# Optimization experiments

Hardware: AMD Instinct MI355X
Metric: run time of the kernel (lower is better)

## Reference

```python
import jax, jax.numpy as jnp
import numpy as np

# Static config (matches init_kwargs: dim=64, ffn=2.66, kernel=3, smk=3, heads=2)
DIM = 64
NUM_HEADS = 2
KS = 3
SMK = 3
POOL = 7           # ContMix pools context to 7x7 -> 49 context tokens
HIDDEN = 172       # round_up(int(64*2.66), 4)
HIDDEN2 = 2 * HIDDEN
CTX_DW = HIDDEN2 // 4   # 86
CTX_DW12 = HIDDEN // 4  # 43
NK = SMK * SMK + KS * KS  # 18


def conv1x1(x, w):
    # x: [B,C,H,W], w: [O,C] -> [B,O,H,W]
    return jnp.einsum('bchw,oc->bohw', x, w)


def extract_patches(x, k):
    # x: [B,C,H,W] -> [B,C,k*k,H,W], zero ('same') padding, stride 1
    p = k // 2
    B, C, H, W = x.shape
    xp = jnp.pad(x, ((0, 0), (0, 0), (p, p), (p, p)))
    pats = [xp[:, :, i:i + H, j:j + W] for i in range(k) for j in range(k)]
    return jnp.stack(pats, axis=2)


def dyn_dw(x, attn, k, heads):
    # Dynamic depthwise mixing: per-pixel, per-head k*k kernel shared across
    # channels within a head. x: [B,C,H,W], attn: [B,g,HW,k*k]
    B, C, H, W = x.shape
    hd = C // heads
    pat = extract_patches(x, k).reshape(B, heads, hd, k * k, H * W)
    out = jnp.einsum('bgdkn,bgnk->bgdn', pat, attn)
    return out.reshape(B, C, H, W)


def contmix(x, ctx, wq, wk, wp, wpb, wo):
    # Content-aware dynamic depthwise-mixing (ContMix, OverLoCK-style).
    B, C, H, W = x.shape
    hd_qk = (C // 2) // NUM_HEADS
    scale = hd_qk ** -0.5
    # query from x, key from 7x7-pooled context
    q = conv1x1(x, wq) * scale                     # [B, C//2, H, W]
    ph, pw = H // POOL, W // POOL
    ctx_p = ctx.reshape(B, -1, POOL, ph, POOL, pw).mean(axis=(3, 5))  # [B,ctx,7,7]
    key = conv1x1(ctx_p, wk)                       # [B, C//2, 7, 7]
    q = q.reshape(B, NUM_HEADS, hd_qk, H * W)
    key = key.reshape(B, NUM_HEADS, hd_qk, POOL * POOL)
    w = jnp.einsum('bgcn,bgcl->bgnl', q, key)      # [B,g,HW,49]
    # project 49 context scores -> smk^2 + k^2 dynamic kernel taps (1x1 conv w/ bias)
    w = jnp.einsum('bgnl,ol->bgno', w, wp) + wpb   # [B,g,HW,18]
    a1 = jax.nn.softmax(w[..., :SMK * SMK], axis=-1)
    a2 = jax.nn.softmax(w[..., SMK * SMK:], axis=-1)
    # first channel half mixed with small kernel, second half with large kernel
    x1, x2 = jnp.split(x, 2, axis=1)
    y = jnp.concatenate([dyn_dw(x1, a1, SMK, NUM_HEADS),
                         dyn_dw(x2, a2, KS, NUM_HEADS)], axis=1)
    return conv1x1(y, wo)


def setup_inputs() -> dict:
    key = jax.random.key(0)
    ks = jax.random.split(key, 32)
    def w(i, o, c):
        return jax.random.normal(ks[i], (o, c), dtype=jnp.float32) / np.sqrt(c)
    inp = {
        'x': jax.random.normal(ks[0], (2, DIM, 112, 112), dtype=jnp.float32),
        'pin_w': w(1, HIDDEN2, DIM),
        'ctx_w': w(2, CTX_DW, HIDDEN2),
        'ctx1_w': w(3, CTX_DW12, HIDDEN),
        'ctx2_w': w(4, CTX_DW12, HIDDEN),
        'pout_w': w(5, DIM, HIDDEN),
        # ContMix on hidden_x2 (dim=344, ctx=86)
        'cm0_q': w(6, HIDDEN2 // 2, HIDDEN2),
        'cm0_k': w(7, HIDDEN2 // 2, CTX_DW),
        'cm0_p': w(8, NK, POOL * POOL),
        'cm0_pb': jnp.zeros((NK,), dtype=jnp.float32),
        'cm0_o': w(9, HIDDEN2, HIDDEN2),
        # ContMix on hidden (dim=172, ctx=43) -- branch 1
        'cm1_q': w(10, HIDDEN // 2, HIDDEN),
        'cm1_k': w(11, HIDDEN // 2, CTX_DW12),
        'cm1_p': w(12, NK, POOL * POOL),
        'cm1_pb': jnp.zeros((NK,), dtype=jnp.float32),
        'cm1_o': w(13, HIDDEN, HIDDEN),
        # ContMix on hidden -- branch 2
        'cm2_q': w(14, HIDDEN // 2, HIDDEN),
        'cm2_k': w(15, HIDDEN // 2, CTX_DW12),
        'cm2_p': w(16, NK, POOL * POOL),
        'cm2_pb': jnp.zeros((NK,), dtype=jnp.float32),
        'cm2_o': w(17, HIDDEN, HIDDEN),
    }
    return inp


def reference(x, pin_w, ctx_w, ctx1_w, ctx2_w, pout_w,
              cm0_q, cm0_k, cm0_p, cm0_pb, cm0_o,
              cm1_q, cm1_k, cm1_p, cm1_pb, cm1_o,
              cm2_q, cm2_k, cm2_p, cm2_pb, cm2_o):
    x_in = conv1x1(x, pin_w)                           # [B, 2*hidden, H, W]
    ctx_dw = conv1x1(x_in, ctx_w)                      # [B, ctx_dw, H, W]
    x_dw = contmix(x_in, ctx_dw, cm0_q, cm0_k, cm0_p, cm0_pb, cm0_o)
    x1, x2 = jnp.split(x_dw, 2, axis=1)                # each [B, hidden, H, W]
    ctx1 = conv1x1(x1, ctx1_w)
    ctx2 = conv1x1(x2, ctx2_w)
    x1p = jnp.tanh(contmix(x1, ctx1, cm1_q, cm1_k, cm1_p, cm1_pb, cm1_o)) + x1
    x2p = jnp.tanh(contmix(x2, ctx2, cm2_q, cm2_k, cm2_p, cm2_pb, cm2_o)) + x2
    out = conv1x1(x1p * x2p, pout_w)                   # [B, dim, H, W]
    return out
```

## Files before the change

kernel.cpp:

```cpp
#include <hip/hip_runtime.h>
#include <math.h>

#define HW 12544
#define W_IMG 112
#define B_SZ 2

typedef __attribute__((ext_vector_type(8))) short s8v;
typedef __attribute__((ext_vector_type(4))) float f4v;

__device__ __forceinline__ void split_bf16(float x, unsigned short& h, unsigned short& l) {
    unsigned u  = __float_as_uint(x);
    unsigned hb = (u + 0x7FFFu + ((u >> 16) & 1u)) >> 16;
    float hf    = __uint_as_float(hb << 16);
    float r     = x - hf;
    unsigned ur = __float_as_uint(r);
    unsigned lb = (ur + 0x7FFFu + ((ur >> 16) & 1u)) >> 16;
    h = (unsigned short)hb; l = (unsigned short)lb;
}

struct WSplitArgs {
    const float* src[8];
    const float* src2[8];
    unsigned short* hi[8];
    unsigned short* lo[8];
    int O1[8]; int O2[8]; int O2B[8]; int K[8]; int Kp[8]; int MpKp[8];
    float scale2[8];
};

__global__ __launch_bounds__(256) void wsplit_k(WSplitArgs a) {
    const int ci  = blockIdx.y;
    const int idx = blockIdx.x * 256 + threadIdx.x;
    if (idx >= a.MpKp[ci]) return;
    const int Kp   = a.Kp[ci];
    const int blk  = 32 * Kp;
    const int mblk = idx / blk;
    const int rem  = idx - mblk * blk;
    const int kc   = rem >> 10;
    const int rem2 = rem & 1023;
    const int kq   = rem2 >> 8;
    const int row  = (rem2 >> 3) & 31;
    const int j    = rem2 & 7;
    const int o = mblk * 32 + row, k = kc * 32 + kq * 8 + j;
    float v = 0.f;
    if (k < a.K[ci]) {
        if (o < a.O1[ci])
            v = a.src[ci][(size_t)o * a.K[ci] + k];
        else if (o >= a.O2B[ci] && o - a.O2B[ci] < a.O2[ci])
            v = a.src2[ci][(size_t)(o - a.O2B[ci]) * a.K[ci] + k] * a.scale2[ci];
    }
    unsigned short h, l;
    split_bf16(v, h, l);
    a.hi[ci][idx] = h; a.lo[ci][idx] = l;
}

__global__ __launch_bounds__(256) void tsplit_k(
    const float* __restrict__ src, size_t bstride, int C, int KC,
    unsigned short* __restrict__ hi, unsigned short* __restrict__ lo)
{
    __shared__ __align__(16) float t[32][36];
    const int b   = blockIdx.z;
    const int hw0 = blockIdx.x * 32;
    const int kc  = blockIdx.y;
    const int c0  = kc * 32;
    const int tid = threadIdx.x;

    {
        const int cl = tid >> 3, hq = (tid & 7) * 4;
        const int c  = c0 + cl;
        float4 v = make_float4(0.f, 0.f, 0.f, 0.f);
        if (c < C)
            v = *(const float4*)(src + (size_t)b * bstride + (size_t)c * HW + hw0 + hq);
        *(float4*)&t[cl][hq] = v;
    }
    __syncthreads();

    const int hl = tid >> 3, cq = (tid & 7) * 4;
    float v0 = t[cq + 0][hl], v1 = t[cq + 1][hl], v2 = t[cq + 2][hl], v3 = t[cq + 3][hl];
    ushort4 h4, l4;
    split_bf16(v0, h4.x, l4.x);
    split_bf16(v1, h4.y, l4.y);
    split_bf16(v2, h4.z, l4.z);
    split_bf16(v3, h4.w, l4.w);
    const int ns = hw0 >> 8, r = (hw0 & 255) + hl;
    const int kq = cq >> 3, j0 = cq & 7;
    const size_t base = (((size_t)b * 49 + ns) * KC + kc) * 8192
                        + (size_t)kq * 2048 + (size_t)r * 8 + j0;
    *(ushort4*)(hi + base) = h4;
    *(ushort4*)(lo + base) = l4;
}

__global__ __launch_bounds__(256) void tsplit2_k(
    const float* __restrict__ src, size_t bstride,
    unsigned short* __restrict__ hi_a, unsigned short* __restrict__ lo_a,
    unsigned short* __restrict__ hi_b, unsigned short* __restrict__ lo_b)
{
    __shared__ __align__(16) float t[32][36];
    const int zz = blockIdx.z, b = zz & 1, br = zz >> 1;
    const int hw0 = blockIdx.x * 32;
    const int kc  = blockIdx.y;
    const int c0  = kc * 32;
    const int tid = threadIdx.x;

    {
        const int cl = tid >> 3, hq = (tid & 7) * 4;
        const int c  = c0 + cl;
        float4 v = make_float4(0.f, 0.f, 0.f, 0.f);
        if (c < 172)
            v = *(const float4*)(src + (size_t)b * bstride
                                 + (size_t)(br * 172 + c) * HW + hw0 + hq);
        *(float4*)&t[cl][hq] = v;
    }
    __syncthreads();

    const int hl = tid >> 3, cq = (tid & 7) * 4;
    float v0 = t[cq + 0][hl], v1 = t[cq + 1][hl], v2 = t[cq + 2][hl], v3 = t[cq + 3][hl];
    ushort4 h4, l4;
    split_bf16(v0, h4.x, l4.x);
    split_bf16(v1, h4.y, l4.y);
    split_bf16(v2, h4.z, l4.z);
    split_bf16(v3, h4.w, l4.w);
    const int ns = hw0 >> 8, r = (hw0 & 255) + hl;
    const int kq = cq >> 3, j0 = cq & 7;
    const size_t base = (((size_t)b * 49 + ns) * 6 + kc) * 8192
                        + (size_t)kq * 2048 + (size_t)r * 8 + j0;
    unsigned short* hi = br ? hi_b : hi_a;
    unsigned short* lo = br ? lo_b : lo_a;
    *(ushort4*)(hi + base) = h4;
    *(ushort4*)(lo + base) = l4;
}

__global__ __launch_bounds__(256) void mulsplit_k(
    const float* __restrict__ t1, const float* __restrict__ t2, size_t bstride,
    unsigned short* __restrict__ hi, unsigned short* __restrict__ lo)
{
    __shared__ __align__(16) float t[32][36];
    const int b   = blockIdx.z;
    const int hw0 = blockIdx.x * 32;
    const int kc  = blockIdx.y;
    const int c0  = kc * 32;
    const int tid = threadIdx.x;

    {
        const int cl = tid >> 3, hq = (tid & 7) * 4;
        const int c  = c0 + cl;
        float4 v = make_float4(0.f, 0.f, 0.f, 0.f);
        if (c < 172) {
            const size_t off = (size_t)b * bstride + (size_t)c * HW + hw0 + hq;
            float4 a = *(const float4*)(t1 + off);
            float4 m = *(const float4*)(t2 + off);
            v = make_float4(a.x * m.x, a.y * m.y, a.z * m.z, a.w * m.w);
        }
        *(float4*)&t[cl][hq] = v;
    }
    __syncthreads();

    const int hl = tid >> 3, cq = (tid & 7) * 4;
    float v0 = t[cq + 0][hl], v1 = t[cq + 1][hl], v2 = t[cq + 2][hl], v3 = t[cq + 3][hl];
    ushort4 h4, l4;
    split_bf16(v0, h4.x, l4.x);
    split_bf16(v1, h4.y, l4.y);
    split_bf16(v2, h4.z, l4.z);
    split_bf16(v3, h4.w, l4.w);
    const int ns = hw0 >> 8, r = (hw0 & 255) + hl;
    const int kq = cq >> 3, j0 = cq & 7;
    const size_t base = (((size_t)b * 49 + ns) * 6 + kc) * 8192
                        + (size_t)kq * 2048 + (size_t)r * 8 + j0;
    *(ushort4*)(hi + base) = h4;
    *(ushort4*)(lo + base) = l4;
}

template <int KP>
__global__ __launch_bounds__(256) void gemm_k(
    const unsigned short* __restrict__ bt_hi, const unsigned short* __restrict__ bt_lo,
    const unsigned short* __restrict__ w_hi,  const unsigned short* __restrict__ w_lo,
    int per_m,
    float* __restrict__ outA, int OA, size_t oa_bstride,
    float* __restrict__ outB, int OB, size_t ob_bstride, int obase)
{
    constexpr int KC = KP / 32;
    __shared__ __align__(16) unsigned short Bh_s[8192];
    __shared__ __align__(16) unsigned short Bl_s[8192];
    __shared__ __align__(16) unsigned short Ah_s[1024];
    __shared__ __align__(16) unsigned short Al_s[1024];

    const int b   = blockIdx.y;
    const int bx  = blockIdx.x;
    const int xcd = bx & 7, t = bx >> 3;
    const int m   = t % per_m;
    const int ns  = (t / per_m) * 8 + xcd;
    if (ns >= 49) return;

    const int tid  = threadIdx.x;
    const int wv   = tid >> 6, lane = tid & 63;
    const int m16  = lane & 15, quad = lane >> 4;
    const int mbase = m * 32;
    const int nbase = ns * 256 + wv * 64;

    const unsigned short* Bh_g = bt_hi + ((size_t)b * 49 + ns) * KC * 8192;
    const unsigned short* Bl_g = bt_lo + ((size_t)b * 49 + ns) * KC * 8192;
    const unsigned short* Ah_g = w_hi + (size_t)m * KC * 1024;
    const unsigned short* Al_g = w_lo + (size_t)m * KC * 1024;

    f4v acc[2][4];
#pragma unroll
    for (int mt = 0; mt < 2; ++mt)
#pragma unroll
        for (int f = 0; f < 4; ++f) acc[mt][f] = (f4v){0.f, 0.f, 0.f, 0.f};

    s8v rB[8], rA;
#pragma unroll
    for (int j = 0; j < 4; ++j) {
        rB[j]     = *(const s8v*)(Bh_g + (size_t)(j * 256 + tid) * 8);
        rB[4 + j] = *(const s8v*)(Bl_g + (size_t)(j * 256 + tid) * 8);
    }
    rA = (tid < 128) ? *(const s8v*)(Ah_g + (size_t)tid * 8)
                     : *(const s8v*)(Al_g + (size_t)(tid - 128) * 8);
#pragma unroll
    for (int j = 0; j < 4; ++j) {
        *(s8v*)(Bh_s + (j * 256 + tid) * 8) = rB[j];
        *(s8v*)(Bl_s + (j * 256 + tid) * 8) = rB[4 + j];
    }
    if (tid < 128) *(s8v*)(Ah_s + tid * 8) = rA;
    else           *(s8v*)(Al_s + (tid - 128) * 8) = rA;
    __syncthreads();

#pragma unroll
    for (int kc = 0; kc < KC; ++kc) {
        if (kc + 1 < KC) {
            const unsigned short* bh = Bh_g + (size_t)(kc + 1) * 8192;
            const unsigned short* bl = Bl_g + (size_t)(kc + 1) * 8192;
#pragma unroll
            for (int j = 0; j < 4; ++j) {
                rB[j]     = *(const s8v*)(bh + (size_t)(j * 256 + tid) * 8);
                rB[4 + j] = *(const s8v*)(bl + (size_t)(j * 256 + tid) * 8);
            }
            rA = (tid < 128)
                ? *(const s8v*)(Ah_g + (size_t)(kc + 1) * 1024 + (size_t)tid * 8)
                : *(const s8v*)(Al_g + (size_t)(kc + 1) * 1024 + (size_t)(tid - 128) * 8);
        }
#pragma unroll
        for (int mt = 0; mt < 2; ++mt) {
            s8v ah = *(const s8v*)(Ah_s + (quad * 32 + mt * 16 + m16) * 8);
            s8v al = *(const s8v*)(Al_s + (quad * 32 + mt * 16 + m16) * 8);
#pragma unroll
            for (int f = 0; f < 4; ++f) {
                const int row = wv * 64 + f * 16 + m16;
                s8v bh = *(const s8v*)(Bh_s + (quad * 256 + row) * 8);
                s8v bl = *(const s8v*)(Bl_s + (quad * 256 + row) * 8);
                acc[mt][f] = __builtin_amdgcn_mfma_f32_16x16x32_bf16(ah, bh, acc[mt][f], 0, 0, 0);
                acc[mt][f] = __builtin_amdgcn_mfma_f32_16x16x32_bf16(al, bh, acc[mt][f], 0, 0, 0);
                acc[mt][f] = __builtin_amdgcn_mfma_f32_16x16x32_bf16(ah, bl, acc[mt][f], 0, 0, 0);
            }
        }
        __syncthreads();
        if (kc + 1 < KC) {
#pragma unroll
            for (int j = 0; j < 4; ++j) {
                *(s8v*)(Bh_s + (j * 256 + tid) * 8) = rB[j];
                *(s8v*)(Bl_s + (j * 256 + tid) * 8) = rB[4 + j];
            }
            if (tid < 128) *(s8v*)(Ah_s + tid * 8) = rA;
            else           *(s8v*)(Al_s + (tid - 128) * 8) = rA;
            __syncthreads();
        }
    }

#pragma unroll
    for (int mt = 0; mt < 2; ++mt) {
#pragma unroll
        for (int f = 0; f < 4; ++f) {
            const int n = nbase + f * 16 + m16;
#pragma unroll
            for (int r = 0; r < 4; ++r) {
                const int o = mbase + mt * 16 + quad * 4 + r;
                float v = acc[mt][f][r];
                if (o < OA) {
                    outA[(size_t)b * oa_bstride + (size_t)o * HW + n] = v;
                } else if (o >= obase && o - obase < OB) {
                    outB[(size_t)b * ob_bstride + (size_t)(o - obase) * HW + n] = v;
                }
            }
        }
    }
}

template <int KP>
__global__ __launch_bounds__(256) void gemm2_k(
    const unsigned short* __restrict__ bth_a, const unsigned short* __restrict__ btl_a,
    const unsigned short* __restrict__ wh_a,  const unsigned short* __restrict__ wl_a,
    const unsigned short* __restrict__ bth_b, const unsigned short* __restrict__ btl_b,
    const unsigned short* __restrict__ wh_b,  const unsigned short* __restrict__ wl_b,
    int per_m,
    float* __restrict__ outA_a, float* __restrict__ outA_b, int OA, size_t oa_bstride,
    float* __restrict__ outB_a, float* __restrict__ outB_b, int OB, size_t ob_bstride, int obase,
    int mode, int Ovalid,
    const float* __restrict__ res_a, const float* __restrict__ res_b, size_t res_bstride)
{
    constexpr int KC = KP / 32;
    __shared__ __align__(16) unsigned short Bh_s[8192];
    __shared__ __align__(16) unsigned short Bl_s[8192];
    __shared__ __align__(16) unsigned short Ah_s[1024];
    __shared__ __align__(16) unsigned short Al_s[1024];

    const int zz  = blockIdx.y, b = zz & 1, br = zz >> 1;
    const int bx  = blockIdx.x;
    const int xcd = bx & 7, t = bx >> 3;
    const int m   = t % per_m;
    const int ns  = (t / per_m) * 8 + xcd;
    if (ns >= 49) return;

    const unsigned short* bt_hi = br ? bth_b : bth_a;
    const unsigned short* bt_lo = br ? btl_b : btl_a;
    const unsigned short* w_hi  = br ? wh_b : wh_a;
    const unsigned short* w_lo  = br ? wl_b : wl_a;
    float* outA = br ? outA_b : outA_a;
    float* outB = br ? outB_b : outB_a;
    const float* res = br ? res_b : res_a;

    const int tid  = threadIdx.x;
    const int wv   = tid >> 6, lane = tid & 63;
    const int m16  = lane & 15, quad = lane >> 4;
    const int mbase = m * 32;
    const int nbase = ns * 256 + wv * 64;

    const unsigned short* Bh_g = bt_hi + ((size_t)b * 49 + ns) * KC * 8192;
    const unsigned short* Bl_g = bt_lo + ((size_t)b * 49 + ns) * KC * 8192;
    const unsigned short* Ah_g = w_hi + (size_t)m * KC * 1024;
    const unsigned short* Al_g = w_lo + (size_t)m * KC * 1024;

    f4v acc[2][4];
#pragma unroll
    for (int mt = 0; mt < 2; ++mt)
#pragma unroll
        for (int f = 0; f < 4; ++f) acc[mt][f] = (f4v){0.f, 0.f, 0.f, 0.f};

    s8v rB[8], rA;
#pragma unroll
    for (int j = 0; j < 4; ++j) {
        rB[j]     = *(const s8v*)(Bh_g + (size_t)(j * 256 + tid) * 8);
        rB[4 + j] = *(const s8v*)(Bl_g + (size_t)(j * 256 + tid) * 8);
    }
    rA = (tid < 128) ? *(const s8v*)(Ah_g + (size_t)tid * 8)
                     : *(const s8v*)(Al_g + (size_t)(tid - 128) * 8);
#pragma unroll
    for (int j = 0; j < 4; ++j) {
        *(s8v*)(Bh_s + (j * 256 + tid) * 8) = rB[j];
        *(s8v*)(Bl_s + (j * 256 + tid) * 8) = rB[4 + j];
    }
    if (tid < 128) *(s8v*)(Ah_s + tid * 8) = rA;
    else           *(s8v*)(Al_s + (tid - 128) * 8) = rA;
    __syncthreads();

#pragma unroll
    for (int kc = 0; kc < KC; ++kc) {
        if (kc + 1 < KC) {
            const unsigned short* bh = Bh_g + (size_t)(kc + 1) * 8192;
            const unsigned short* bl = Bl_g + (size_t)(kc + 1) * 8192;
#pragma unroll
            for (int j = 0; j < 4; ++j) {
                rB[j]     = *(const s8v*)(bh + (size_t)(j * 256 + tid) * 8);
                rB[4 + j] = *(const s8v*)(bl + (size_t)(j * 256 + tid) * 8);
            }
            rA = (tid < 128)
                ? *(const s8v*)(Ah_g + (size_t)(kc + 1) * 1024 + (size_t)tid * 8)
                : *(const s8v*)(Al_g + (size_t)(kc + 1) * 1024 + (size_t)(tid - 128) * 8);
        }
#pragma unroll
        for (int mt = 0; mt < 2; ++mt) {
            s8v ah = *(const s8v*)(Ah_s + (quad * 32 + mt * 16 + m16) * 8);
            s8v al = *(const s8v*)(Al_s + (quad * 32 + mt * 16 + m16) * 8);
#pragma unroll
            for (int f = 0; f < 4; ++f) {
                const int row = wv * 64 + f * 16 + m16;
                s8v bh = *(const s8v*)(Bh_s + (quad * 256 + row) * 8);
                s8v bl = *(const s8v*)(Bl_s + (quad * 256 + row) * 8);
                acc[mt][f] = __builtin_amdgcn_mfma_f32_16x16x32_bf16(ah, bh, acc[mt][f], 0, 0, 0);
                acc[mt][f] = __builtin_amdgcn_mfma_f32_16x16x32_bf16(al, bh, acc[mt][f], 0, 0, 0);
                acc[mt][f] = __builtin_amdgcn_mfma_f32_16x16x32_bf16(ah, bl, acc[mt][f], 0, 0, 0);
            }
        }
        __syncthreads();
        if (kc + 1 < KC) {
#pragma unroll
            for (int j = 0; j < 4; ++j) {
                *(s8v*)(Bh_s + (j * 256 + tid) * 8) = rB[j];
                *(s8v*)(Bl_s + (j * 256 + tid) * 8) = rB[4 + j];
            }
            if (tid < 128) *(s8v*)(Ah_s + tid * 8) = rA;
            else           *(s8v*)(Al_s + (tid - 128) * 8) = rA;
            __syncthreads();
        }
    }

#pragma unroll
    for (int mt = 0; mt < 2; ++mt) {
#pragma unroll
        for (int f = 0; f < 4; ++f) {
            const int n = nbase + f * 16 + m16;
#pragma unroll
            for (int r = 0; r < 4; ++r) {
                const int o = mbase + mt * 16 + quad * 4 + r;
                float v = acc[mt][f][r];
                if (mode == 2 && o < Ovalid)
                    v = tanhf(v) + res[(size_t)b * res_bstride + (size_t)o * HW + n];
                if (o < OA) {
                    outA[(size_t)b * oa_bstride + (size_t)o * HW + n] = v;
                } else if (o >= obase && o - obase < OB) {
                    outB[(size_t)b * ob_bstride + (size_t)(o - obase) * HW + n] = v;
                }
            }
        }
    }
}

__global__ __launch_bounds__(256) void dyndw_bt_k(
    const float* __restrict__ x, const float* __restrict__ attn,
    unsigned short* __restrict__ hi, unsigned short* __restrict__ lo,
    int C, int C_half, int hd, size_t x_bstride, int KC)
{
    const int b  = blockIdx.z, ns = blockIdx.x, tid = threadIdx.x;
    const int c0 = blockIdx.y * 8;
    const int hw = ns * 256 + tid;
    const int h = hw / W_IMG, w = hw - h * W_IMG;

    int off[9]; bool val[9];
#pragma unroll
    for (int i = 0; i < 3; ++i)
#pragma unroll
        for (int j = 0; j < 3; ++j) {
            const int hh = h + i - 1, ww = w + j - 1;
            val[i * 3 + j] = (hh >= 0 && hh < 112 && ww >= 0 && ww < 112);
            off[i * 3 + j] = hh * W_IMG + ww;
        }

    s8v hvv, lvv;
#pragma unroll
    for (int u = 0; u < 8; ++u) {
        const int c = c0 + u;
        float acc = 0.f;
        if (c < C) {
            const int half = c / C_half;
            const int g = (c - half * C_half) / hd;
            const float* ap = attn + ((size_t)(b * 2 + g) * 18 + half * 9) * HW + hw;
            const float* xp = x + (size_t)b * x_bstride + (size_t)c * HW;
#pragma unroll
            for (int k = 0; k < 9; ++k) {
                const float xv = val[k] ? xp[off[k]] : 0.f;
                acc += ap[(size_t)k * HW] * xv;
            }
        }
        unsigned short hs, ls;
        split_bf16(acc, hs, ls);
        hvv[u] = (short)hs; lvv[u] = (short)ls;
    }

    const int kc = c0 >> 5, kq = (c0 & 31) >> 3;
    const size_t base = (((size_t)b * 49 + ns) * KC + kc) * 8192
                        + (size_t)kq * 2048 + (size_t)tid * 8;
    *(s8v*)(hi + base) = hvv;
    *(s8v*)(lo + base) = lvv;
}

__global__ __launch_bounds__(256) void dyndw2_bt_k(
    const float* __restrict__ x, size_t x_bstride,
    const float* __restrict__ attn_a, const float* __restrict__ attn_b,
    unsigned short* __restrict__ hi_a, unsigned short* __restrict__ lo_a,
    unsigned short* __restrict__ hi_b, unsigned short* __restrict__ lo_b)
{
    const int zz = blockIdx.z, b = zz & 1, br = zz >> 1;
    const int ns = blockIdx.x, tid = threadIdx.x;
    const int c0 = blockIdx.y * 8;
    const int hw = ns * 256 + tid;
    const int h = hw / W_IMG, w = hw - h * W_IMG;

    const float* attn = br ? attn_b : attn_a;
    unsigned short* hi = br ? hi_b : hi_a;
    unsigned short* lo = br ? lo_b : lo_a;

    int off[9]; bool val[9];
#pragma unroll
    for (int i = 0; i < 3; ++i)
#pragma unroll
        for (int j = 0; j < 3; ++j) {
            const int hh = h + i - 1, ww = w + j - 1;
            val[i * 3 + j] = (hh >= 0 && hh < 112 && ww >= 0 && ww < 112);
            off[i * 3 + j] = hh * W_IMG + ww;
        }

    s8v hvv, lvv;
#pragma unroll
    for (int u = 0; u < 8; ++u) {
        const int c = c0 + u;
        float acc = 0.f;
        if (c < 172) {
            const int half = c / 86;
            const int g = (c - half * 86) / 43;
            const float* ap = attn + ((size_t)(b * 2 + g) * 18 + half * 9) * HW + hw;
            const float* xp = x + (size_t)b * x_bstride + (size_t)(br * 172 + c) * HW;
#pragma unroll
            for (int k = 0; k < 9; ++k) {
                const float xv = val[k] ? xp[off[k]] : 0.f;
                acc += ap[(size_t)k * HW] * xv;
            }
        }
        unsigned short hs, ls;
        split_bf16(acc, hs, ls);
        hvv[u] = (short)hs; lvv[u] = (short)ls;
    }

    const int kc = c0 >> 5, kq = (c0 & 31) >> 3;
    const size_t base = (((size_t)b * 49 + ns) * 6 + kc) * 8192
                        + (size_t)kq * 2048 + (size_t)tid * 8;
    *(s8v*)(hi + base) = hvv;
    *(s8v*)(lo + base) = lvv;
}

__global__ __launch_bounds__(64) void pool_k(
    const float* __restrict__ ctx, float* __restrict__ pooled, int C)
{
    const int c = blockIdx.x, b = blockIdx.y, t = threadIdx.x;
    if (t >= 49) return;
    const int ph = t / 7, pw = t % 7;
    const float* src = ctx + ((size_t)b * C + c) * HW;
    float sum = 0.f;
    for (int i = 0; i < 16; ++i) {
        const float* row = src + (ph * 16 + i) * W_IMG + pw * 16;
        for (int j = 0; j < 16; ++j) sum += row[j];
    }
    pooled[((size_t)b * C + c) * 49 + t] = sum * (1.0f / 256.0f);
}

__global__ __launch_bounds__(64) void pool2_k(
    const float* __restrict__ ctx_a, const float* __restrict__ ctx_b,
    float* __restrict__ p_a, float* __restrict__ p_b, int C)
{
    const int zz = blockIdx.y, b = zz & 1, br = zz >> 1;
    const int c = blockIdx.x, t = threadIdx.x;
    if (t >= 49) return;
    const float* ctx = br ? ctx_b : ctx_a;
    float* pooled    = br ? p_b : p_a;
    const int ph = t / 7, pw = t % 7;
    const float* src = ctx + ((size_t)b * C + c) * HW;
    float sum = 0.f;
    for (int i = 0; i < 16; ++i) {
        const float* row = src + (ph * 16 + i) * W_IMG + pw * 16;
        for (int j = 0; j < 16; ++j) sum += row[j];
    }
    pooled[((size_t)b * C + c) * 49 + t] = sum * (1.0f / 256.0f);
}

__global__ __launch_bounds__(64) void keygemm_k(
    const float* __restrict__ pooled, const float* __restrict__ wk,
    float* __restrict__ key, int K, int O)
{
    const int o = blockIdx.x, b = blockIdx.y, l = threadIdx.x;
    if (l >= 49) return;
    float s = 0.f;
    for (int c = 0; c < K; ++c)
        s += wk[(size_t)o * K + c] * pooled[((size_t)b * K + c) * 49 + l];
    key[((size_t)b * O + o) * 49 + l] = s;
}

__global__ __launch_bounds__(64) void keygemm2_k(
    const float* __restrict__ p_a, const float* __restrict__ p_b,
    const float* __restrict__ wk_a, const float* __restrict__ wk_b,
    float* __restrict__ k_a, float* __restrict__ k_b, int K, int O)
{
    const int zz = blockIdx.y, b = zz & 1, br = zz >> 1;
    const int o = blockIdx.x, l = threadIdx.x;
    if (l >= 49) return;
    const float* pooled = br ? p_b : p_a;
    const float* wk     = br ? wk_b : wk_a;
    float* key          = br ? k_b : k_a;
    float s = 0.f;
    for (int c = 0; c < K; ++c)
        s += wk[(size_t)o * K + c] * pooled[((size_t)b * K + c) * 49 + l];
    key[((size_t)b * O + o) * 49 + l] = s;
}

__device__ __forceinline__ void attn_body(
    const float* __restrict__ q, const float* __restrict__ key,
    const float* __restrict__ wp, const float* __restrict__ pb,
    float* __restrict__ attn, int hd, int b, int g, int tid, int nsx)
{
    __shared__ float klds[86 * 52];
    __shared__ float plds[18 * 52];
    __shared__ float pblds[18];

    for (int idx = tid; idx < hd * 49; idx += 256) {
        int c = idx / 49, l = idx - c * 49;
        klds[c * 52 + l] = key[((size_t)(b * 2 + g) * hd + c) * 49 + l];
    }
    for (int idx = tid; idx < hd * 3; idx += 256) {
        int c = idx / 3;
        klds[c * 52 + 49 + (idx - c * 3)] = 0.f;
    }
    for (int idx = tid; idx < 18 * 49; idx += 256) {
        int o = idx / 49, l = idx - o * 49;
        plds[o * 52 + l] = wp[o * 49 + l];
    }
    for (int idx = tid; idx < 18 * 3; idx += 256) {
        int o = idx / 3;
        plds[o * 52 + 49 + (idx - o * 3)] = 0.f;
    }
    if (tid < 18) pblds[tid] = pb[tid];
    __syncthreads();

    const int hw = nsx * 256 + tid;

    float4 s[13];
#pragma unroll
    for (int t = 0; t < 13; ++t) s[t] = make_float4(0.f, 0.f, 0.f, 0.f);

    const float* qp = q + (size_t)(b * 2 + g) * hd * HW + hw;
    for (int c = 0; c < hd; ++c) {
        float qv = qp[(size_t)c * HW];
        const float4* kr = (const float4*)(klds + c * 52);
#pragma unroll
        for (int t = 0; t < 13; ++t) {
            float4 kv = kr[t];
            s[t].x += qv * kv.x; s[t].y += qv * kv.y;
            s[t].z += qv * kv.z; s[t].w += qv * kv.w;
        }
    }

    float e[18];
#pragma unroll
    for (int o = 0; o < 18; ++o) {
        const float4* pr = (const float4*)(plds + o * 52);
        float4 a = make_float4(0.f, 0.f, 0.f, 0.f);
#pragma unroll
        for (int t = 0; t < 13; ++t) {
            float4 pv = pr[t];
            a.x += s[t].x * pv.x; a.y += s[t].y * pv.y;
            a.z += s[t].z * pv.z; a.w += s[t].w * pv.w;
        }
        e[o] = pblds[o] + a.x + a.y + a.z + a.w;
    }

    float* outp = attn + (size_t)(b * 2 + g) * 18 * HW + hw;
#pragma unroll
    for (int half = 0; half < 2; ++half) {
        int base = half * 9;
        float m = e[base];
#pragma unroll
        for (int k = 1; k < 9; ++k) m = fmaxf(m, e[base + k]);
        float sum = 0.f, ex[9];
#pragma unroll
        for (int k = 0; k < 9; ++k) { ex[k] = expf(e[base + k] - m); sum += ex[k]; }
        float inv = 1.0f / sum;
#pragma unroll
        for (int k = 0; k < 9; ++k) outp[(size_t)(base + k) * HW] = ex[k] * inv;
    }
}

__global__ __launch_bounds__(256) void attn_k(
    const float* __restrict__ q, const float* __restrict__ key,
    const float* __restrict__ wp, const float* __restrict__ pb,
    float* __restrict__ attn, int hd)
{
    attn_body(q, key, wp, pb, attn, hd, blockIdx.z, blockIdx.y, threadIdx.x, blockIdx.x);
}

__global__ __launch_bounds__(256) void attn2_k(
    const float* __restrict__ q_a, const float* __restrict__ q_b,
    const float* __restrict__ k_a, const float* __restrict__ k_b,
    const float* __restrict__ wp_a, const float* __restrict__ wp_b,
    const float* __restrict__ pb_a, const float* __restrict__ pb_b,
    float* __restrict__ at_a, float* __restrict__ at_b, int hd)
{
    const int zz = blockIdx.z, b = zz & 1, br = zz >> 1;
    attn_body(br ? q_b : q_a, br ? k_b : k_a, br ? wp_b : wp_a,
              br ? pb_b : pb_a, br ? at_b : at_a, hd, b, blockIdx.y,
              threadIdx.x, blockIdx.x);
}

extern "C" void kernel_launch(void* const* d_in, const int* in_sizes, int n_in,
                              void* d_out, int out_size, void* d_ws, size_t ws_size,
                              hipStream_t stream) {
    const float* x      = (const float*)d_in[0];
    const float* pin_w  = (const float*)d_in[1];
    const float* ctx_w  = (const float*)d_in[2];
    const float* ctx1_w = (const float*)d_in[3];
    const float* ctx2_w = (const float*)d_in[4];
    const float* pout_w = (const float*)d_in[5];
    const float* cm0_q  = (const float*)d_in[6];
    const float* cm0_k  = (const float*)d_in[7];
    const float* cm0_p  = (const float*)d_in[8];
    const float* cm0_pb = (const float*)d_in[9];
    const float* cm0_o  = (const float*)d_in[10];
    const float* cm1_q  = (const float*)d_in[11];
    const float* cm1_k  = (const float*)d_in[12];
    const float* cm1_p  = (const float*)d_in[13];
    const float* cm1_pb = (const float*)d_in[14];
    const float* cm1_o  = (const float*)d_in[15];
    const float* cm2_q  = (const float*)d_in[16];
    const float* cm2_k  = (const float*)d_in[17];
    const float* cm2_p  = (const float*)d_in[18];
    const float* cm2_pb = (const float*)d_in[19];
    const float* cm2_o  = (const float*)d_in[20];
    float* out = (float*)d_out;

    float* ws = (float*)d_ws;
    float* x_in  = ws;
    float* t1    = ws;
    float* t2    = ws + 8630272;
    float* x_dw  = ws + 17260544;
    float* ctxb  = ws + 25890816;
    float* ctx1  = ws + 28048384;
    float* ctx2  = ws + 29127168;
    float* q0    = ws + 30205952;
    float* q1    = ws + 30205952;
    float* q2    = ws + 32363520;
    float* attn0 = ws + 34521088;
    float* attn1 = ws + 35424256;
    float* attn2 = ws + 36327424;
    float* pool0 = ws + 37230592;
    float* pool1 = ws + 37239020;
    float* pool2b= ws + 37243234;
    float* key0  = ws + 37247448;
    float* key1  = ws + 37264304;
    float* key2  = ws + 37272732;
    unsigned short* ub = (unsigned short*)(ws + 37281160);
    static const int WOFF[8] = {0, 45056, 247808, 518144, 579584, 641024, 714752, 788480};
    static const int WO1[8]  = {344, 86, 172, 43, 43, 172, 172, 64};
    static const int WO2[8]  = {0, 172, 172, 86, 86, 0, 0, 0};
    static const int O2B[8]  = {352, 86, 192, 43, 43, 192, 192, 64};
    static const int WK[8]   = {64, 344, 344, 172, 172, 172, 172, 172};
    static const int WKP[8]  = {64, 352, 352, 192, 192, 192, 192, 192};
    static const int WMP[8]  = {352, 288, 384, 160, 160, 192, 192, 64};
    unsigned short* xt_hi   = ub + 813056;
    unsigned short* xt_lo   = ub + 2418688;
    unsigned short* bigA_hi = ub + 4024320;
    unsigned short* bigA_lo = ub + 12855296;
    unsigned short* x1t_hi  = ub + 21686272;
    unsigned short* x1t_lo  = ub + 26503168;
    unsigned short* x2t_hi  = ub + 31320064;
    unsigned short* x2t_lo  = ub + 36136960;

    const float sc0 = 1.0f / sqrtf(86.0f);
    const float sc1 = 1.0f / sqrtf(43.0f);
    const size_t BS344 = (size_t)344 * HW, BS172 = (size_t)172 * HW,
                 BS86 = (size_t)86 * HW, BS64 = (size_t)64 * HW, BS43 = (size_t)43 * HW;

    WSplitArgs wa;
    const float* wsrc1[8] = {pin_w, ctx_w, cm0_o, ctx1_w, ctx2_w, cm1_o, cm2_o, pout_w};
    const float* wsrc2[8] = {nullptr, cm0_q, cm0_o + (size_t)172 * 344, cm1_q, cm2_q,
                             nullptr, nullptr, nullptr};
    const float wsc2[8]   = {1.f, sc0, 1.f, sc1, sc1, 1.f, 1.f, 1.f};
    for (int i = 0; i < 8; ++i) {
        wa.src[i] = wsrc1[i]; wa.src2[i] = wsrc2[i];
        wa.hi[i]  = ub + WOFF[i];
        wa.lo[i]  = ub + WOFF[i] + WMP[i] * WKP[i];
        wa.O1[i] = WO1[i]; wa.O2[i] = WO2[i]; wa.O2B[i] = O2B[i];
        wa.K[i] = WK[i]; wa.Kp[i] = WKP[i];
        wa.MpKp[i] = WMP[i] * WKP[i];
        wa.scale2[i] = wsc2[i];
    }
    wsplit_k<<<dim3(528, 8), 256, 0, stream>>>(wa);

#define WHI(CI) (ub + WOFF[CI])
#define WLO(CI) (ub + WOFF[CI] + WMP[CI] * WKP[CI])
#define GRID(CI) dim3((WMP[CI] / 32) * 56, B_SZ)
#define GRID2(CI) dim3((WMP[CI] / 32) * 56, 2 * B_SZ)

    tsplit_k<<<dim3(392, 2, B_SZ), 256, 0, stream>>>(x, BS64, 64, 2, xt_hi, xt_lo);
    gemm_k<64><<<GRID(0), 256, 0, stream>>>(
        xt_hi, xt_lo, WHI(0), WLO(0), WMP[0] / 32,
        x_in, 344, BS344, nullptr, 0, 0, 352);
    tsplit_k<<<dim3(392, 11, B_SZ), 256, 0, stream>>>(x_in, BS344, 344, 11, bigA_hi, bigA_lo);

    gemm_k<352><<<GRID(1), 256, 0, stream>>>(
        bigA_hi, bigA_lo, WHI(1), WLO(1), WMP[1] / 32,
        ctxb, 86, BS86, q0, 172, BS172, 86);
    pool_k<<<dim3(86, B_SZ), dim3(64), 0, stream>>>(ctxb, pool0, 86);
    keygemm_k<<<dim3(172, B_SZ), dim3(64), 0, stream>>>(pool0, cm0_k, key0, 86, 172);
    attn_k<<<dim3(49, 2, B_SZ), dim3(256), 0, stream>>>(q0, key0, cm0_p, cm0_pb, attn0, 86);
    dyndw_bt_k<<<dim3(49, 44, B_SZ), 256, 0, stream>>>(
        x_in, attn0, bigA_hi, bigA_lo, 344, 172, 86, BS344, 11);
    gemm_k<352><<<GRID(2), 256, 0, stream>>>(
        bigA_hi, bigA_lo, WHI(2), WLO(2), WMP[2] / 32,
        x_dw, 172, BS344, x_dw + BS172, 172, BS344, 192);

    tsplit2_k<<<dim3(392, 6, 2 * B_SZ), 256, 0, stream>>>(
        x_dw, BS344, x1t_hi, x1t_lo, x2t_hi, x2t_lo);

    gemm2_k<192><<<GRID2(3), 256, 0, stream>>>(
        x1t_hi, x1t_lo, WHI(3), WLO(3),
        x2t_hi, x2t_lo, WHI(4), WLO(4), WMP[3] / 32,
        ctx1, ctx2, 43, BS43,
        q1, q2, 86, BS86, 43,
        0, 129, nullptr, nullptr, 0);
    pool2_k<<<dim3(43, 2 * B_SZ), dim3(64), 0, stream>>>(ctx1, ctx2, pool1, pool2b, 43);
    keygemm2_k<<<dim3(86, 2 * B_SZ), dim3(64), 0, stream>>>(
        pool1, pool2b, cm1_k, cm2_k, key1, key2, 43, 86);
    attn2_k<<<dim3(49, 2, 2 * B_SZ), dim3(256), 0, stream>>>(
        q1, q2, key1, key2, cm1_p, cm2_p, cm1_pb, cm2_pb, attn1, attn2, 43);
    dyndw2_bt_k<<<dim3(49, 24, 2 * B_SZ), 256, 0, stream>>>(
        x_dw, BS344, attn1, attn2, x1t_hi, x1t_lo, x2t_hi, x2t_lo);
    gemm2_k<192><<<GRID2(5), 256, 0, stream>>>(
        x1t_hi, x1t_lo, WHI(5), WLO(5),
        x2t_hi, x2t_lo, WHI(6), WLO(6), WMP[5] / 32,
        t1, t2, 172, BS172,
        nullptr, nullptr, 0, 0, 192,
        2, 172, x_dw, x_dw + BS172, BS344);

    mulsplit_k<<<dim3(392, 6, B_SZ), 256, 0, stream>>>(t1, t2, BS172, bigA_hi, bigA_lo);

    gemm_k<192><<<GRID(7), 256, 0, stream>>>(
        bigA_hi, bigA_lo, WHI(7), WLO(7), WMP[7] / 32,
        out, 64, BS64, nullptr, 0, 0, 64);

#undef WHI
#undef WLO
#undef GRID
#undef GRID2
}
```

Measured before the change: 487.2 us.

## Widen gemm2 M-tile to 64 rows and fuse key projection into attention

The dual-branch GEMM kernel now computes 64 output rows per block instead of 32. Each block reuses its staged activation tile across twice as many weight rows, which halves the number of blocks that reload the large B operand. Padding for the ctx/q weights grows from 160 to 192 rows to fit the new tile. Separately, the key projection kernels are removed and the key is computed from the pooled context inside the attention kernel. This saves launches and a round trip through memory, but every attention block redundantly recomputes the small key matrix.

```diff
diff --git a/kernel.cpp b/kernel.cpp
--- a/kernel.cpp
+++ b/kernel.cpp
@@ -299,8 +299,8 @@
     constexpr int KC = KP / 32;
     __shared__ __align__(16) unsigned short Bh_s[8192];
     __shared__ __align__(16) unsigned short Bl_s[8192];
-    __shared__ __align__(16) unsigned short Ah_s[1024];
-    __shared__ __align__(16) unsigned short Al_s[1024];
+    __shared__ __align__(16) unsigned short Ah_s[4096];
+    __shared__ __align__(16) unsigned short Al_s[4096];
 
     const int zz  = blockIdx.y, b = zz & 1, br = zz >> 1;
     const int bx  = blockIdx.x;
@@ -320,35 +320,37 @@
     const int tid  = threadIdx.x;
     const int wv   = tid >> 6, lane = tid & 63;
     const int m16  = lane & 15, quad = lane >> 4;
-    const int mbase = m * 32;
+    const int mbase = m * 64;
     const int nbase = ns * 256 + wv * 64;
 
     const unsigned short* Bh_g = bt_hi + ((size_t)b * 49 + ns) * KC * 8192;
     const unsigned short* Bl_g = bt_lo + ((size_t)b * 49 + ns) * KC * 8192;
-    const unsigned short* Ah_g = w_hi + (size_t)m * KC * 1024;
-    const unsigned short* Al_g = w_lo + (size_t)m * KC * 1024;
-
-    f4v acc[2][4];
-#pragma unroll
-    for (int mt = 0; mt < 2; ++mt)
+    const int amb = tid >> 7;
+    const int aoff = (tid & 127) * 8;
+    const unsigned short* Ah_g = w_hi + (size_t)(2 * m + amb) * KC * 1024 + aoff;
+    const unsigned short* Al_g = w_lo + (size_t)(2 * m + amb) * KC * 1024 + aoff;
+
+    f4v acc[4][4];
+#pragma unroll
+    for (int mt = 0; mt < 4; ++mt)
 #pragma unroll
         for (int f = 0; f < 4; ++f) acc[mt][f] = (f4v){0.f, 0.f, 0.f, 0.f};
 
-    s8v rB[8], rA;
+    s8v rB[8], rA[2];
 #pragma unroll
     for (int j = 0; j < 4; ++j) {
         rB[j]     = *(const s8v*)(Bh_g + (size_t)(j * 256 + tid) * 8);
         rB[4 + j] = *(const s8v*)(Bl_g + (size_t)(j * 256 + tid) * 8);
     }
-    rA = (tid < 128) ? *(const s8v*)(Ah_g + (size_t)tid * 8)
-                     : *(const s8v*)(Al_g + (size_t)(tid - 128) * 8);
+    rA[0] = *(const s8v*)(Ah_g);
+    rA[1] = *(const s8v*)(Al_g);
 #pragma unroll
     for (int j = 0; j < 4; ++j) {
         *(s8v*)(Bh_s + (j * 256 + tid) * 8) = rB[j];
         *(s8v*)(Bl_s + (j * 256 + tid) * 8) = rB[4 + j];
     }
-    if (tid < 128) *(s8v*)(Ah_s + tid * 8) = rA;
-    else           *(s8v*)(Al_s + (tid - 128) * 8) = rA;
+    *(s8v*)(Ah_s + amb * 2048 + aoff) = rA[0];
+    *(s8v*)(Al_s + amb * 2048 + aoff) = rA[1];
     __syncthreads();
 
 #pragma unroll
@@ -361,14 +363,14 @@
                 rB[j]     = *(const s8v*)(bh + (size_t)(j * 256 + tid) * 8);
                 rB[4 + j] = *(const s8v*)(bl + (size_t)(j * 256 + tid) * 8);
             }
-            rA = (tid < 128)
-                ? *(const s8v*)(Ah_g + (size_t)(kc + 1) * 1024 + (size_t)tid * 8)
-                : *(const s8v*)(Al_g + (size_t)(kc + 1) * 1024 + (size_t)(tid - 128) * 8);
-        }
-#pragma unroll
-        for (int mt = 0; mt < 2; ++mt) {
-            s8v ah = *(const s8v*)(Ah_s + (quad * 32 + mt * 16 + m16) * 8);
-            s8v al = *(const s8v*)(Al_s + (quad * 32 + mt * 16 + m16) * 8);
+            rA[0] = *(const s8v*)(Ah_g + (size_t)(kc + 1) * 1024);
+            rA[1] = *(const s8v*)(Al_g + (size_t)(kc + 1) * 1024);
+        }
+#pragma unroll
+        for (int mt = 0; mt < 4; ++mt) {
+            const int ab = (mt >> 1) * 2048 + (quad * 32 + (mt & 1) * 16 + m16) * 8;
+            s8v ah = *(const s8v*)(Ah_s + ab);
+            s8v al = *(const s8v*)(Al_s + ab);
 #pragma unroll
             for (int f = 0; f < 4; ++f) {
                 const int row = wv * 64 + f * 16 + m16;
@@ -386,14 +388,14 @@
                 *(s8v*)(Bh_s + (j * 256 + tid) * 8) = rB[j];
                 *(s8v*)(Bl_s + (j * 256 + tid) * 8) = rB[4 + j];
             }
-            if (tid < 128) *(s8v*)(Ah_s + tid * 8) = rA;
-            else           *(s8v*)(Al_s + (tid - 128) * 8) = rA;
+            *(s8v*)(Ah_s + amb * 2048 + aoff) = rA[0];
+            *(s8v*)(Al_s + amb * 2048 + aoff) = rA[1];
             __syncthreads();
         }
     }
 
 #pragma unroll
-    for (int mt = 0; mt < 2; ++mt) {
+    for (int mt = 0; mt < 4; ++mt) {
 #pragma unroll
         for (int f = 0; f < 4; ++f) {
             const int n = nbase + f * 16 + m16;
@@ -549,39 +551,11 @@
     pooled[((size_t)b * C + c) * 49 + t] = sum * (1.0f / 256.0f);
 }
 
-__global__ __launch_bounds__(64) void keygemm_k(
-    const float* __restrict__ pooled, const float* __restrict__ wk,
-    float* __restrict__ key, int K, int O)
-{
-    const int o = blockIdx.x, b = blockIdx.y, l = threadIdx.x;
-    if (l >= 49) return;
-    float s = 0.f;
-    for (int c = 0; c < K; ++c)
-        s += wk[(size_t)o * K + c] * pooled[((size_t)b * K + c) * 49 + l];
-    key[((size_t)b * O + o) * 49 + l] = s;
-}
-
-__global__ __launch_bounds__(64) void keygemm2_k(
-    const float* __restrict__ p_a, const float* __restrict__ p_b,
-    const float* __restrict__ wk_a, const float* __restrict__ wk_b,
-    float* __restrict__ k_a, float* __restrict__ k_b, int K, int O)
-{
-    const int zz = blockIdx.y, b = zz & 1, br = zz >> 1;
-    const int o = blockIdx.x, l = threadIdx.x;
-    if (l >= 49) return;
-    const float* pooled = br ? p_b : p_a;
-    const float* wk     = br ? wk_b : wk_a;
-    float* key          = br ? k_b : k_a;
-    float s = 0.f;
-    for (int c = 0; c < K; ++c)
-        s += wk[(size_t)o * K + c] * pooled[((size_t)b * K + c) * 49 + l];
-    key[((size_t)b * O + o) * 49 + l] = s;
-}
-
 __device__ __forceinline__ void attn_body(
-    const float* __restrict__ q, const float* __restrict__ key,
+    const float* __restrict__ q, const float* __restrict__ pooled,
+    const float* __restrict__ wk,
     const float* __restrict__ wp, const float* __restrict__ pb,
-    float* __restrict__ attn, int hd, int b, int g, int tid, int nsx)
+    float* __restrict__ attn, int hd, int K, int b, int g, int tid, int nsx)
 {
     __shared__ float klds[86 * 52];
     __shared__ float plds[18 * 52];
@@ -589,7 +563,11 @@
 
     for (int idx = tid; idx < hd * 49; idx += 256) {
         int c = idx / 49, l = idx - c * 49;
-        klds[c * 52 + l] = key[((size_t)(b * 2 + g) * hd + c) * 49 + l];
+        const float* wkr = wk + (size_t)(g * hd + c) * K;
+        const float* pl  = pooled + (size_t)b * K * 49 + l;
+        float s = 0.f;
+        for (int k = 0; k < K; ++k) s += wkr[k] * pl[(size_t)k * 49];
+        klds[c * 52 + l] = s;
     }
     for (int idx = tid; idx < hd * 3; idx += 256) {
         int c = idx / 3;
@@ -655,24 +633,26 @@
 }
 
 __global__ __launch_bounds__(256) void attn_k(
-    const float* __restrict__ q, const float* __restrict__ key,
-    const float* __restrict__ wp, const float* __restrict__ pb,
-    float* __restrict__ attn, int hd)
-{
-    attn_body(q, key, wp, pb, attn, hd, blockIdx.z, blockIdx.y, threadIdx.x, blockIdx.x);
+    const float* __restrict__ q, const float* __restrict__ pooled,
+    const float* __restrict__ wk, const float* __restrict__ wp,
+    const float* __restrict__ pb, float* __restrict__ attn, int hd, int K)
+{
+    attn_body(q, pooled, wk, wp, pb, attn, hd, K,
+              blockIdx.z, blockIdx.y, threadIdx.x, blockIdx.x);
 }
 
 __global__ __launch_bounds__(256) void attn2_k(
     const float* __restrict__ q_a, const float* __restrict__ q_b,
-    const float* __restrict__ k_a, const float* __restrict__ k_b,
+    const float* __restrict__ p_a, const float* __restrict__ p_b,
+    const float* __restrict__ wk_a, const float* __restrict__ wk_b,
     const float* __restrict__ wp_a, const float* __restrict__ wp_b,
     const float* __restrict__ pb_a, const float* __restrict__ pb_b,
-    float* __restrict__ at_a, float* __restrict__ at_b, int hd)
+    float* __restrict__ at_a, float* __restrict__ at_b, int hd, int K)
 {
     const int zz = blockIdx.z, b = zz & 1, br = zz >> 1;
-    attn_body(br ? q_b : q_a, br ? k_b : k_a, br ? wp_b : wp_a,
-              br ? pb_b : pb_a, br ? at_b : at_a, hd, b, blockIdx.y,
-              threadIdx.x, blockIdx.x);
+    attn_body(br ? q_b : q_a, br ? p_b : p_a, br ? wk_b : wk_a,
+              br ? wp_b : wp_a, br ? pb_b : pb_a, br ? at_b : at_a,
+              hd, K, b, blockIdx.y, threadIdx.x, blockIdx.x);
 }
 
 extern "C" void kernel_launch(void* const* d_in, const int* in_sizes, int n_in,
@@ -718,25 +698,22 @@
     float* pool0 = ws + 37230592;
     float* pool1 = ws + 37239020;
     float* pool2b= ws + 37243234;
-    float* key0  = ws + 37247448;
-    float* key1  = ws + 37264304;
-    float* key2  = ws + 37272732;
-    unsigned short* ub = (unsigned short*)(ws + 37281160);
-    static const int WOFF[8] = {0, 45056, 247808, 518144, 579584, 641024, 714752, 788480};
+    unsigned short* ub = (unsigned short*)(ws + 37247448);
+    static const int WOFF[8] = {0, 45056, 247808, 518144, 591872, 665600, 739328, 813056};
     static const int WO1[8]  = {344, 86, 172, 43, 43, 172, 172, 64};
     static const int WO2[8]  = {0, 172, 172, 86, 86, 0, 0, 0};
     static const int O2B[8]  = {352, 86, 192, 43, 43, 192, 192, 64};
     static const int WK[8]   = {64, 344, 344, 172, 172, 172, 172, 172};
     static const int WKP[8]  = {64, 352, 352, 192, 192, 192, 192, 192};
-    static const int WMP[8]  = {352, 288, 384, 160, 160, 192, 192, 64};
-    unsigned short* xt_hi   = ub + 813056;
-    unsigned short* xt_lo   = ub + 2418688;
-    unsigned short* bigA_hi = ub + 4024320;
-    unsigned short* bigA_lo = ub + 12855296;
-    unsigned short* x1t_hi  = ub + 21686272;
-    unsigned short* x1t_lo  = ub + 26503168;
-    unsigned short* x2t_hi  = ub + 31320064;
-    unsigned short* x2t_lo  = ub + 36136960;
+    static const int WMP[8]  = {352, 288, 384, 192, 192, 192, 192, 64};
+    unsigned short* xt_hi   = ub + 837632;
+    unsigned short* xt_lo   = ub + 2443264;
+    unsigned short* bigA_hi = ub + 4048896;
+    unsigned short* bigA_lo = ub + 12879872;
+    unsigned short* x1t_hi  = ub + 21710848;
+    unsigned short* x1t_lo  = ub + 26527744;
+    unsigned short* x2t_hi  = ub + 31344640;
+    unsigned short* x2t_lo  = ub + 36161536;
 
     const float sc0 = 1.0f / sqrtf(86.0f);
     const float sc1 = 1.0f / sqrtf(43.0f);
@@ -762,7 +739,7 @@
 #define WHI(CI) (ub + WOFF[CI])
 #define WLO(CI) (ub + WOFF[CI] + WMP[CI] * WKP[CI])
 #define GRID(CI) dim3((WMP[CI] / 32) * 56, B_SZ)
-#define GRID2(CI) dim3((WMP[CI] / 32) * 56, 2 * B_SZ)
+#define GRID2_64(CI) dim3((WMP[CI] / 64) * 56, 2 * B_SZ)
 
     tsplit_k<<<dim3(392, 2, B_SZ), 256, 0, stream>>>(x, BS64, 64, 2, xt_hi, xt_lo);
     gemm_k<64><<<GRID(0), 256, 0, stream>>>(
@@ -774,8 +751,8 @@
         bigA_hi, bigA_lo, WHI(1), WLO(1), WMP[1] / 32,
         ctxb, 86, BS86, q0, 172, BS172, 86);
     pool_k<<<dim3(86, B_SZ), dim3(64), 0, stream>>>(ctxb, pool0, 86);
-    keygemm_k<<<dim3(172, B_SZ), dim3(64), 0, stream>>>(pool0, cm0_k, key0, 86, 172);
-    attn_k<<<dim3(49, 2, B_SZ), dim3(256), 0, stream>>>(q0, key0, cm0_p, cm0_pb, attn0, 86);
+    attn_k<<<dim3(49, 2, B_SZ), dim3(256), 0, stream>>>(
+        q0, pool0, cm0_k, cm0_p, cm0_pb, attn0, 86, 86);
     dyndw_bt_k<<<dim3(49, 44, B_SZ), 256, 0, stream>>>(
         x_in, attn0, bigA_hi, bigA_lo, 344, 172, 86, BS344, 11);
     gemm_k<352><<<GRID(2), 256, 0, stream>>>(
@@ -785,22 +762,21 @@
     tsplit2_k<<<dim3(392, 6, 2 * B_SZ), 256, 0, stream>>>(
         x_dw, BS344, x1t_hi, x1t_lo, x2t_hi, x2t_lo);
 
-    gemm2_k<192><<<GRID2(3), 256, 0, stream>>>(
+    gemm2_k<192><<<GRID2_64(3), 256, 0, stream>>>(
         x1t_hi, x1t_lo, WHI(3), WLO(3),
-        x2t_hi, x2t_lo, WHI(4), WLO(4), WMP[3] / 32,
+        x2t_hi, x2t_lo, WHI(4), WLO(4), WMP[3] / 64,
         ctx1, ctx2, 43, BS43,
         q1, q2, 86, BS86, 43,
         0, 129, nullptr, nullptr, 0);
     pool2_k<<<dim3(43, 2 * B_SZ), dim3(64), 0, stream>>>(ctx1, ctx2, pool1, pool2b, 43);
-    keygemm2_k<<<dim3(86, 2 * B_SZ), dim3(64), 0, stream>>>(
-        pool1, pool2b, cm1_k, cm2_k, key1, key2, 43, 86);
     attn2_k<<<dim3(49, 2, 2 * B_SZ), dim3(256), 0, stream>>>(
-        q1, q2, key1, key2, cm1_p, cm2_p, cm1_pb, cm2_pb, attn1, attn2, 43);
+        q1, q2, pool1, pool2b, cm1_k, cm2_k, cm1_p, cm2_p,
+        cm1_pb, cm2_pb, attn1, attn2, 43, 43);
     dyndw2_bt_k<<<dim3(49, 24, 2 * B_SZ), 256, 0, stream>>>(
         x_dw, BS344, attn1, attn2, x1t_hi, x1t_lo, x2t_hi, x2t_lo);
-    gemm2_k<192><<<GRID2(5), 256, 0, stream>>>(
+    gemm2_k<192><<<GRID2_64(5), 256, 0, stream>>>(
         x1t_hi, x1t_lo, WHI(5), WLO(5),
-        x2t_hi, x2t_lo, WHI(6), WLO(6), WMP[5] / 32,
+        x2t_hi, x2t_lo, WHI(6), WLO(6), WMP[5] / 64,
         t1, t2, 172, BS172,
         nullptr, nullptr, 0, 0, 192,
         2, 172, x_dw, x_dw + BS172, BS344);
@@ -814,5 +790,5 @@
 #undef WHI
 #undef WLO
 #undef GRID
-#undef GRID2
-}
+#undef GRID2_64
+}
```

After: 593.0 us. 21.7% more time.
